# Performance work log

Measured on AMD Instinct MI355X. Metric: run time of the kernel, lower is better.

## Reference

```python
import jax, jax.numpy as jnp
import numpy as np

H = W = 512
NUM_RINGS = 256  # min(image_shape) // 2
B = 128

def _make_bins():
    # Mirrors the torch __init__: fftshift=True, rfft=False
    center = np.array([H // 2, W // 2], dtype=np.float32)
    ii, jj = np.meshgrid(np.arange(H), np.arange(W), indexing='ij')
    coords = np.stack([ii, jj], -1).astype(np.float32) - center
    r = np.sqrt((coords ** 2).sum(-1))
    bins = np.round(r).astype(np.int32).reshape(-1)          # [H*W]
    mask = (bins > 3) & (bins < NUM_RINGS)                   # valid_bins_mask
    return bins, mask

def setup_inputs() -> dict:
    key = jax.random.key(0)
    k1, k2 = jax.random.split(key)
    parts = jax.random.normal(k1, (B, H, W), dtype=jnp.float32)
    projs = jax.random.normal(k2, (B, H, W), dtype=jnp.float32)
    bins, mask = _make_bins()
    return {
        "parts": parts,
        "projs": projs,
        "distance_bins": jnp.asarray(bins),
        "valid_mask": jnp.asarray(mask),
        "num_segments": int(bins.max()) + 1,  # static python int (= 363)
    }

def reference(parts, projs, distance_bins, valid_mask, num_segments):
    b = parts.shape[0]
    noise = (parts - projs).reshape(b, -1)                    # [B, H*W]
    a = jnp.abs(noise)

    seg = lambda x: jax.ops.segment_sum(x, distance_bins, num_segments=num_segments)
    counts = seg(jnp.ones(distance_bins.shape, jnp.float32))  # [NS], same for all batch rows

    # scatter_std (unbiased=True) ** 2 -> per-bin variance, two-pass
    sum_a = jax.vmap(seg)(a)                                  # [B, NS]
    mean = sum_a / jnp.maximum(counts, 1.0)[None, :]
    dev = a - mean[:, distance_bins]                          # gather mean back to pixels
    ssq = jax.vmap(seg)(dev * dev)                            # [B, NS]
    radial_var = ssq / jnp.maximum(counts - 1.0, 1.0)[None, :]

    flat_var = radial_var[:, distance_bins]                   # gather-broadcast [B, H*W]
    exp_term = -0.5 * (noise * noise) / flat_var
    logprob = exp_term - jnp.log(2.0 * jnp.pi * flat_var)
    logprob = jnp.where(valid_mask[None, :], logprob, 0.0).sum(-1, keepdims=True)  # [B, 1]
    return logprob
```

## Files before the change

kernel.cpp:

```cpp
#include <hip/hip_runtime.h>

#define HW (512 * 512)
#define NBINS 256
#define NB 128
#define NTILES 64
#define TPX 4096


__global__ __launch_bounds__(256) void tilesort(const int* __restrict__ bins,
                                                int* __restrict__ perm,
                                                int* __restrict__ tileCount,
                                                int* __restrict__ counts) {
    __shared__ int hist[NBINS];
    __shared__ int sc[NBINS];
    __shared__ int cursor[NBINS];
    const int t = threadIdx.x;
    const int tile = blockIdx.x;
    const int trow = tile >> 3, tcol = tile & 7;
    hist[t] = 0;
    __syncthreads();

    int myBins[16];
    #pragma unroll
    for (int k = 0; k < 4; ++k) {
        int row = (t >> 4) + k * 16;
        int col4 = t & 15;
        int4 v = *(const int4*)&bins[(trow * 64 + row) * 512 + tcol * 64 + col4 * 4];
        int bb[4] = {v.x, v.y, v.z, v.w};
        #pragma unroll
        for (int m = 0; m < 4; ++m) {
            myBins[k * 4 + m] = bb[m];
            if (bb[m] > 3 && bb[m] < NBINS) atomicAdd(&hist[bb[m]], 1);
        }
    }
    __syncthreads();
    sc[t] = hist[t];
    __syncthreads();
    for (int off = 1; off < 256; off <<= 1) {
        int x = (t >= off) ? sc[t - off] : 0;
        __syncthreads();
        sc[t] += x;
        __syncthreads();
    }
    cursor[t] = sc[t] - hist[t];
    if (t == 255) tileCount[tile] = sc[255];
    if (hist[t]) atomicAdd(&counts[t], hist[t]);
    __syncthreads();

    #pragma unroll
    for (int k = 0; k < 4; ++k) {
        int row = (t >> 4) + k * 16;
        int col4 = t & 15;
        #pragma unroll
        for (int m = 0; m < 4; ++m) {
            int bn = myBins[k * 4 + m];
            if (bn > 3 && bn < NBINS) {
                int local = row * 64 + col4 * 4 + m;
                int pos = atomicAdd(&cursor[bn], 1);
                perm[tile * TPX + pos] = (bn << 12) | local;
            }
        }
    }
}

__global__ __launch_bounds__(256) void pass(const float* __restrict__ parts,
                                            const float* __restrict__ projs,
                                            const int* __restrict__ perm,
                                            const int* __restrict__ tileCount,
                                            float* __restrict__ S1,
                                            float* __restrict__ S2) {
    __shared__ float sP[TPX], sQ[TPX];
    __shared__ float h1[NBINS], h2[NBINS];
    const int t = threadIdx.x;
    const int tile = blockIdx.x;
    const int b = blockIdx.y;
    const int trow = tile >> 3, tcol = tile & 7;
    h1[t] = 0.f; h2[t] = 0.f;

    const float* __restrict__ P = parts + (size_t)b * HW;
    const float* __restrict__ Q = projs + (size_t)b * HW;

    #pragma unroll
    for (int k = 0; k < 4; ++k) {
        int row = (t >> 4) + k * 16;
        int col4 = t & 15;
        const float4 p = *(const float4*)&P[(trow * 64 + row) * 512 + tcol * 64 + col4 * 4];
        const float4 q = *(const float4*)&Q[(trow * 64 + row) * 512 + tcol * 64 + col4 * 4];
        int x = row & 31;
        int rb = row * 64;
        sP[rb + ((col4 * 4 + 0) ^ x)] = p.x;
        sP[rb + ((col4 * 4 + 1) ^ x)] = p.y;
        sP[rb + ((col4 * 4 + 2) ^ x)] = p.z;
        sP[rb + ((col4 * 4 + 3) ^ x)] = p.w;
        sQ[rb + ((col4 * 4 + 0) ^ x)] = q.x;
        sQ[rb + ((col4 * 4 + 1) ^ x)] = q.y;
        sQ[rb + ((col4 * 4 + 2) ^ x)] = q.z;
        sQ[rb + ((col4 * 4 + 3) ^ x)] = q.w;
    }
    __syncthreads();

    const int count = tileCount[tile];
    const int e0 = t * 16;
    float a1 = 0.f, a2 = 0.f;
    int curBin = -1;

    if (e0 < count) {
        const int4* pe = (const int4*)(perm + tile * TPX + e0);
        #pragma unroll
        for (int g = 0; g < 4; ++g) {
            int4 e4 = pe[g];
            int ee[4] = {e4.x, e4.y, e4.z, e4.w};
            #pragma unroll
            for (int k2 = 0; k2 < 4; ++k2) {
                int idx = e0 + g * 4 + k2;
                if (idx < count) {
                    int e = ee[k2];
                    int bn = e >> 12;
                    int local = e & 4095;
                    int slot = local ^ ((local >> 6) & 31);
                    float n = sP[slot] - sQ[slot];
                    if (bn != curBin) {
                        if (curBin >= 0) {
                            atomicAdd(&h1[curBin], a1);
                            atomicAdd(&h2[curBin], a2);
                        }
                        curBin = bn; a1 = 0.f; a2 = 0.f;
                    }
                    a1 += fabsf(n);
                    a2 += n * n;
                }
            }
        }
        if (curBin >= 0) {
            atomicAdd(&h1[curBin], a1);
            atomicAdd(&h2[curBin], a2);
        }
    }
    __syncthreads();
    if (h1[t] != 0.f) unsafeAtomicAdd(&S1[b * NBINS + t], h1[t]);
    if (h2[t] != 0.f) unsafeAtomicAdd(&S2[b * NBINS + t], h2[t]);
}

__global__ __launch_bounds__(256) void finalize(const float* __restrict__ S1,
                                                const float* __restrict__ S2,
                                                const int* __restrict__ counts,
                                                float* __restrict__ out) {
    const int b = blockIdx.x;
    const int t = threadIdx.x;
    float contrib = 0.f;
    if (t > 3) {
        float c = (float)counts[t];
        float s1 = S1[b * NBINS + t];
        float s2 = S2[b * NBINS + t];
        float mean = s1 / fmaxf(c, 1.f);
        float ssq = fmaxf(s2 - mean * s1, 0.f);
        float var = ssq / fmaxf(c - 1.f, 1.f);
        contrib = -0.5f * s2 / var - c * logf(6.283185307179586f * var);
    }
    #pragma unroll
    for (int off = 32; off > 0; off >>= 1) contrib += __shfl_down(contrib, off, 64);
    __shared__ float w[4];
    if ((t & 63) == 0) w[t >> 6] = contrib;
    __syncthreads();
    if (t == 0) out[b] = w[0] + w[1] + w[2] + w[3];
}

extern "C" void kernel_launch(void* const* d_in, const int* in_sizes, int n_in,
                              void* d_out, int out_size, void* d_ws, size_t ws_size,
                              hipStream_t stream) {
    const float* parts = (const float*)d_in[0];
    const float* projs = (const float*)d_in[1];
    const int* bins    = (const int*)d_in[2];
    float* out = (float*)d_out;

    char* ws = (char*)d_ws;
    int*   tileCount = (int*)(ws + 0);
    int*   counts    = (int*)(ws + 512);
    float* S1        = (float*)(ws + 4096);
    float* S2        = (float*)(ws + 135168);
    int*   perm      = (int*)(ws + 266240);

    hipMemsetAsync(d_ws, 0, 266240, stream);

    tilesort<<<NTILES, 256, 0, stream>>>(bins, perm, tileCount, counts);
    pass    <<<dim3(NTILES, NB), 256, 0, stream>>>(parts, projs, perm, tileCount, S1, S2);
    finalize<<<NB, 256, 0, stream>>>(S1, S2, counts, out);
}
```

Before: 306.9 us.

## Replace tile-sorted permutation with direct shared-memory atomic histogramming

Drops the tile sort that built a bin-sorted permutation, and the LDS staging of each tile that the pass kernel used. The pass kernel now streams parts, projs and bins linearly in 8192-pixel chunks and does per-element LDS atomicAdd into per-bin accumulators. This removes the permutation writes and reads, the prefix scan and the LDS staging, but it adds per-pixel LDS float atomics with contention on neighbouring pixels that share a bin. It also reads the bins array once per batch row instead of the permutation.

```diff
diff --git a/kernel.cpp b/kernel.cpp
--- a/kernel.cpp
+++ b/kernel.cpp
@@ -3,142 +3,68 @@
 #define HW (512 * 512)
 #define NBINS 256
 #define NB 128
-#define NTILES 64
-#define TPX 4096
+#define CHUNKS 32
+#define CPX4 2048
 
 
-__global__ __launch_bounds__(256) void tilesort(const int* __restrict__ bins,
-                                                int* __restrict__ perm,
-                                                int* __restrict__ tileCount,
-                                                int* __restrict__ counts) {
+__global__ __launch_bounds__(256) void countk(const int* __restrict__ bins,
+                                              int* __restrict__ counts) {
     __shared__ int hist[NBINS];
-    __shared__ int sc[NBINS];
-    __shared__ int cursor[NBINS];
     const int t = threadIdx.x;
-    const int tile = blockIdx.x;
-    const int trow = tile >> 3, tcol = tile & 7;
     hist[t] = 0;
     __syncthreads();
-
-    int myBins[16];
+    const int4* __restrict__ B4 = (const int4*)bins + blockIdx.x * CPX4;
     #pragma unroll
-    for (int k = 0; k < 4; ++k) {
-        int row = (t >> 4) + k * 16;
-        int col4 = t & 15;
-        int4 v = *(const int4*)&bins[(trow * 64 + row) * 512 + tcol * 64 + col4 * 4];
-        int bb[4] = {v.x, v.y, v.z, v.w};
-        #pragma unroll
-        for (int m = 0; m < 4; ++m) {
-            myBins[k * 4 + m] = bb[m];
-            if (bb[m] > 3 && bb[m] < NBINS) atomicAdd(&hist[bb[m]], 1);
-        }
+    for (int g = 0; g < 8; ++g) {
+        int4 bb = B4[g * 256 + t];
+        if (bb.x > 3 && bb.x < NBINS) atomicAdd(&hist[bb.x], 1);
+        if (bb.y > 3 && bb.y < NBINS) atomicAdd(&hist[bb.y], 1);
+        if (bb.z > 3 && bb.z < NBINS) atomicAdd(&hist[bb.z], 1);
+        if (bb.w > 3 && bb.w < NBINS) atomicAdd(&hist[bb.w], 1);
     }
     __syncthreads();
-    sc[t] = hist[t];
-    __syncthreads();
-    for (int off = 1; off < 256; off <<= 1) {
-        int x = (t >= off) ? sc[t - off] : 0;
-        __syncthreads();
-        sc[t] += x;
-        __syncthreads();
-    }
-    cursor[t] = sc[t] - hist[t];
-    if (t == 255) tileCount[tile] = sc[255];
     if (hist[t]) atomicAdd(&counts[t], hist[t]);
-    __syncthreads();
-
-    #pragma unroll
-    for (int k = 0; k < 4; ++k) {
-        int row = (t >> 4) + k * 16;
-        int col4 = t & 15;
-        #pragma unroll
-        for (int m = 0; m < 4; ++m) {
-            int bn = myBins[k * 4 + m];
-            if (bn > 3 && bn < NBINS) {
-                int local = row * 64 + col4 * 4 + m;
-                int pos = atomicAdd(&cursor[bn], 1);
-                perm[tile * TPX + pos] = (bn << 12) | local;
-            }
-        }
-    }
 }
 
 __global__ __launch_bounds__(256) void pass(const float* __restrict__ parts,
                                             const float* __restrict__ projs,
-                                            const int* __restrict__ perm,
-                                            const int* __restrict__ tileCount,
+                                            const int* __restrict__ bins,
                                             float* __restrict__ S1,
                                             float* __restrict__ S2) {
-    __shared__ float sP[TPX], sQ[TPX];
     __shared__ float h1[NBINS], h2[NBINS];
     const int t = threadIdx.x;
-    const int tile = blockIdx.x;
+    const int chunk = blockIdx.x;
     const int b = blockIdx.y;
-    const int trow = tile >> 3, tcol = tile & 7;
-    h1[t] = 0.f; h2[t] = 0.f;
+    h1[t] = 0.f;
+    h2[t] = 0.f;
+    __syncthreads();
 
-    const float* __restrict__ P = parts + (size_t)b * HW;
-    const float* __restrict__ Q = projs + (size_t)b * HW;
+    const float4* __restrict__ P4 = (const float4*)(parts + (size_t)b * HW) + chunk * CPX4;
+    const float4* __restrict__ Q4 = (const float4*)(projs + (size_t)b * HW) + chunk * CPX4;
+    const int4*   __restrict__ B4 = (const int4*)bins + chunk * CPX4;
 
-    #pragma unroll
-    for (int k = 0; k < 4; ++k) {
-        int row = (t >> 4) + k * 16;
-        int col4 = t & 15;
-        const float4 p = *(const float4*)&P[(trow * 64 + row) * 512 + tcol * 64 + col4 * 4];
-        const float4 q = *(const float4*)&Q[(trow * 64 + row) * 512 + tcol * 64 + col4 * 4];
-        int x = row & 31;
-        int rb = row * 64;
-        sP[rb + ((col4 * 4 + 0) ^ x)] = p.x;
-        sP[rb + ((col4 * 4 + 1) ^ x)] = p.y;
-        sP[rb + ((col4 * 4 + 2) ^ x)] = p.z;
-        sP[rb + ((col4 * 4 + 3) ^ x)] = p.w;
-        sQ[rb + ((col4 * 4 + 0) ^ x)] = q.x;
-        sQ[rb + ((col4 * 4 + 1) ^ x)] = q.y;
-        sQ[rb + ((col4 * 4 + 2) ^ x)] = q.z;
-        sQ[rb + ((col4 * 4 + 3) ^ x)] = q.w;
+    #pragma unroll 2
+    for (int g = 0; g < 8; ++g) {
+        const int idx = g * 256 + t;
+        const float4 p = P4[idx];
+        const float4 q = Q4[idx];
+        const int4  bb = B4[idx];
+        float n;
+        n = p.x - q.x;
+        if (bb.x > 3 && bb.x < NBINS) { atomicAdd(&h1[bb.x], fabsf(n)); atomicAdd(&h2[bb.x], n * n); }
+        n = p.y - q.y;
+        if (bb.y > 3 && bb.y < NBINS) { atomicAdd(&h1[bb.y], fabsf(n)); atomicAdd(&h2[bb.y], n * n); }
+        n = p.z - q.z;
+        if (bb.z > 3 && bb.z < NBINS) { atomicAdd(&h1[bb.z], fabsf(n)); atomicAdd(&h2[bb.z], n * n); }
+        n = p.w - q.w;
+        if (bb.w > 3 && bb.w < NBINS) { atomicAdd(&h1[bb.w], fabsf(n)); atomicAdd(&h2[bb.w], n * n); }
     }
     __syncthreads();
 
-    const int count = tileCount[tile];
-    const int e0 = t * 16;
-    float a1 = 0.f, a2 = 0.f;
-    int curBin = -1;
-
-    if (e0 < count) {
-        const int4* pe = (const int4*)(perm + tile * TPX + e0);
-        #pragma unroll
-        for (int g = 0; g < 4; ++g) {
-            int4 e4 = pe[g];
-            int ee[4] = {e4.x, e4.y, e4.z, e4.w};
-            #pragma unroll
-            for (int k2 = 0; k2 < 4; ++k2) {
-                int idx = e0 + g * 4 + k2;
-                if (idx < count) {
-                    int e = ee[k2];
-                    int bn = e >> 12;
-                    int local = e & 4095;
-                    int slot = local ^ ((local >> 6) & 31);
-                    float n = sP[slot] - sQ[slot];
-                    if (bn != curBin) {
-                        if (curBin >= 0) {
-                            atomicAdd(&h1[curBin], a1);
-                            atomicAdd(&h2[curBin], a2);
-                        }
-                        curBin = bn; a1 = 0.f; a2 = 0.f;
-                    }
-                    a1 += fabsf(n);
-                    a2 += n * n;
-                }
-            }
-        }
-        if (curBin >= 0) {
-            atomicAdd(&h1[curBin], a1);
-            atomicAdd(&h2[curBin], a2);
-        }
-    }
-    __syncthreads();
-    if (h1[t] != 0.f) unsafeAtomicAdd(&S1[b * NBINS + t], h1[t]);
-    if (h2[t] != 0.f) unsafeAtomicAdd(&S2[b * NBINS + t], h2[t]);
+    const float v1 = h1[t];
+    const float v2 = h2[t];
+    if (v1 != 0.f) unsafeAtomicAdd(&S1[b * NBINS + t], v1);
+    if (v2 != 0.f) unsafeAtomicAdd(&S2[b * NBINS + t], v2);
 }
 
 __global__ __launch_bounds__(256) void finalize(const float* __restrict__ S1,
@@ -174,15 +100,12 @@
     float* out = (float*)d_out;
 
     char* ws = (char*)d_ws;
-    int*   tileCount = (int*)(ws + 0);
-    int*   counts    = (int*)(ws + 512);
-    float* S1        = (float*)(ws + 4096);
-    float* S2        = (float*)(ws + 135168);
-    int*   perm      = (int*)(ws + 266240);
+    int*   counts = (int*)(ws + 0);
+    float* S1     = (float*)(ws + 1024);
+    float* S2     = (float*)(ws + 132096);
 
-    hipMemsetAsync(d_ws, 0, 266240, stream);
-
-    tilesort<<<NTILES, 256, 0, stream>>>(bins, perm, tileCount, counts);
-    pass    <<<dim3(NTILES, NB), 256, 0, stream>>>(parts, projs, perm, tileCount, S1, S2);
+    hipMemsetAsync(d_ws, 0, 263168, stream);
+    countk  <<<CHUNKS, 256, 0, stream>>>(bins, counts);
+    pass    <<<dim3(CHUNKS, NB), 256, 0, stream>>>(parts, projs, bins, S1, S2);
     finalize<<<NB, 256, 0, stream>>>(S1, S2, counts, out);
 }
```

Measured after the change: 526.4 us. 1.72x slower.
